# Optimization experiments

Hardware: AMD Instinct MI355X
Metric: run time of the kernel (lower is better)

The kernel has to match this reference:

```python
import jax, jax.numpy as jnp
import numpy as np

N_NODES = 40000
N_EDGES = 640000
D_FEAT = 128
HIDDEN = 128
N_GRAPHS = 512


def setup_inputs() -> dict:
    key = jax.random.key(0)
    ks = jax.random.split(key, 6)
    x = jax.random.normal(ks[0], (N_NODES, D_FEAT), dtype=jnp.float32)
    edge_index = jax.random.randint(ks[1], (2, N_EDGES), 0, N_NODES, dtype=jnp.int32)
    batch = jnp.sort(jax.random.randint(ks[2], (N_NODES,), 0, N_GRAPHS, dtype=jnp.int32))
    s1 = 1.0 / np.sqrt(D_FEAT)
    s2 = 1.0 / np.sqrt(HIDDEN)
    W1 = jax.random.normal(ks[3], (D_FEAT, HIDDEN), dtype=jnp.float32) * s1
    b1 = jnp.zeros((HIDDEN,), dtype=jnp.float32)
    W2 = jax.random.normal(ks[4], (HIDDEN, HIDDEN), dtype=jnp.float32) * s2
    b2 = jnp.zeros((HIDDEN,), dtype=jnp.float32)
    Wfc = jax.random.normal(ks[5], (HIDDEN, 1), dtype=jnp.float32) * s2
    bfc = jnp.zeros((1,), dtype=jnp.float32)
    return {"x": x, "edge_index": edge_index, "batch": batch,
            "W1": W1, "b1": b1, "W2": W2, "b2": b2, "Wfc": Wfc, "bfc": bfc}


def _gcn_conv(x, edge_index, W, b):
    # PyG GCNConv: linear transform, add self-loops, symmetric deg^{-1/2} norm,
    # scatter-add messages from row (source) to col (target), then bias.
    n = x.shape[0]
    h = x @ W  # [N, H]
    row, col = edge_index[0], edge_index[1]
    ones = jnp.ones_like(col, dtype=h.dtype)
    deg = 1.0 + jax.ops.segment_sum(ones, col, num_segments=n)  # self-loop included
    dinv = jax.lax.rsqrt(deg)  # [N]
    norm = dinv[row] * dinv[col]  # [E]
    msg = h[row] * norm[:, None]  # [E, H]
    out = jax.ops.segment_sum(msg, col, num_segments=n)
    out = out + h * (dinv * dinv)[:, None]  # self-loop contribution
    return out + b


def _mean_pool(x, batch, num_graphs):
    sums = jax.ops.segment_sum(x, batch, num_segments=num_graphs)
    cnt = jax.ops.segment_sum(jnp.ones((x.shape[0],), dtype=x.dtype), batch, num_segments=num_graphs)
    return sums / jnp.maximum(cnt, 1.0)[:, None]


def reference(x, edge_index, batch, W1, b1, W2, b2, Wfc, bfc):
    h = jax.nn.relu(_gcn_conv(x, edge_index, W1, b1))
    h = jax.nn.relu(_gcn_conv(h, edge_index, W2, b2))
    g = _mean_pool(h, batch, N_GRAPHS)  # [G, H]
    return g @ Wfc + bfc  # [G, 1]
```

## Files before the change

kernel.cpp:

```cpp
#include <hip/hip_runtime.h>

#define N_NODES 40000
#define N_EDGES 640000
#define NFEAT   128
#define N_GRAPHS 512
#define SCAN_NB 157


__global__ void edge_deg_int_kernel(const int* __restrict__ ei, int* __restrict__ degcnt, int E) {
    int e = blockIdx.x * blockDim.x + threadIdx.x;
    if (e < E) atomicAdd(&degcnt[ei[E + e]], 1);
}

__global__ void dinv_from_int_kernel(const int* __restrict__ degcnt, float* __restrict__ dinv, int n) {
    int i = blockIdx.x * blockDim.x + threadIdx.x;
    if (i < n) dinv[i] = rsqrtf(1.0f + (float)degcnt[i]);
}

__global__ void scan1_kernel(const int* __restrict__ in, int* __restrict__ out,
                             int* __restrict__ bsums, float* __restrict__ dinv, int n) {
    __shared__ int tmp[256];
    int t = threadIdx.x;
    int i = blockIdx.x * 256 + t;
    int v = (i < n) ? in[i] : 0;
    if (i < n) dinv[i] = rsqrtf(1.0f + (float)v);
    tmp[t] = v;
    __syncthreads();
    for (int off = 1; off < 256; off <<= 1) {
        int add = (t >= off) ? tmp[t - off] : 0;
        __syncthreads();
        tmp[t] += add;
        __syncthreads();
    }
    if (i < n) out[i] = tmp[t] - v;
    if (t == 255) bsums[blockIdx.x] = tmp[255];
}

__global__ void scan2_kernel(int* __restrict__ bsums, int nb) {
    __shared__ int tmp[256];
    int t = threadIdx.x;
    int v = (t < nb) ? bsums[t] : 0;
    tmp[t] = v;
    __syncthreads();
    for (int off = 1; off < 256; off <<= 1) {
        int add = (t >= off) ? tmp[t - off] : 0;
        __syncthreads();
        tmp[t] += add;
        __syncthreads();
    }
    if (t < nb) bsums[t] = tmp[t] - v;
}

__global__ void scan3_kernel(int* __restrict__ rowptr, const int* __restrict__ bsums,
                             int* __restrict__ cursor, int n, int E) {
    int i = blockIdx.x * 256 + threadIdx.x;
    if (i < n) {
        int v = rowptr[i] + bsums[blockIdx.x];
        rowptr[i] = v;
        cursor[i] = v;
    }
    if (i == 0) rowptr[n] = E;
}

template <typename IdxT>
__global__ void fill_kernel(const int* __restrict__ ei, int* __restrict__ cursor,
                            IdxT* __restrict__ csr, int E) {
    int e = blockIdx.x * blockDim.x + threadIdx.x;
    if (e < E) {
        int c = ei[E + e];
        int p = atomicAdd(&cursor[c], 1);
        csr[p] = (IdxT)ei[e];
    }
}

__global__ __launch_bounds__(256, 4) void gemm64_kernel(const float* __restrict__ X,
                                                        const float* __restrict__ W,
                                                        const float* __restrict__ dinv,
                                                        float* __restrict__ H) {
    __shared__ float Ws[128 * 64];
    const int colhalf = blockIdx.x & 1;
    const int tile    = blockIdx.x >> 1;

    for (int i = threadIdx.x; i < 2048; i += 256) {
        int k   = i >> 4;
        int cc4 = (i & 15) * 4;
        *(float4*)(Ws + k * 64 + cc4) = *(const float4*)(W + k * 128 + colhalf * 64 + cc4);
    }
    __syncthreads();

    const int rg = threadIdx.x >> 4;
    const int cg = threadIdx.x & 15;
    const int row0 = tile * 64 + rg * 4;
    const float* x0 = X + (size_t)row0 * NFEAT;

    float acc[4][4] = {};
    float4 xc[4], xn[4];
    #pragma unroll
    for (int i = 0; i < 4; i++) xc[i] = *(const float4*)(x0 + (size_t)i * NFEAT);

    #pragma unroll 4
    for (int k = 0; k < 128; k += 4) {
        const int kn = (k + 4) & 127;
        #pragma unroll
        for (int i = 0; i < 4; i++) xn[i] = *(const float4*)(x0 + (size_t)i * NFEAT + kn);

        float4 wv[4];
        #pragma unroll
        for (int m = 0; m < 4; m++) wv[m] = *(const float4*)(Ws + (k + m) * 64 + cg * 4);

        #pragma unroll
        for (int i = 0; i < 4; i++) {
            const float xi[4] = {xc[i].x, xc[i].y, xc[i].z, xc[i].w};
            #pragma unroll
            for (int m = 0; m < 4; m++) {
                acc[i][0] += xi[m] * wv[m].x;
                acc[i][1] += xi[m] * wv[m].y;
                acc[i][2] += xi[m] * wv[m].z;
                acc[i][3] += xi[m] * wv[m].w;
            }
        }
        #pragma unroll
        for (int i = 0; i < 4; i++) xc[i] = xn[i];
    }

    #pragma unroll
    for (int i = 0; i < 4; i++) {
        float dr = dinv[row0 + i];
        float4 o = {acc[i][0] * dr, acc[i][1] * dr, acc[i][2] * dr, acc[i][3] * dr};
        *(float4*)(H + (size_t)(row0 + i) * NFEAT + colhalf * 64 + cg * 4) = o;
    }
}

template <typename IdxT>
__global__ __launch_bounds__(256) void gather4_kernel(const int* __restrict__ rowptr,
                                                      const IdxT* __restrict__ csr,
                                                      const float* __restrict__ dinv,
                                                      const float* __restrict__ Ht,
                                                      const float* __restrict__ bias,
                                                      float* __restrict__ out, int n) {
    int gid  = blockIdx.x * blockDim.x + threadIdx.x;
    int node = gid >> 6;
    if (node >= n) return;
    int lane = threadIdx.x & 63;
    int half = lane >> 5;
    int f4   = (lane & 31) * 4;

    int start = rowptr[node];
    int end   = rowptr[node + 1];

    float4 a0 = {0.f, 0.f, 0.f, 0.f};
    float4 a1 = {0.f, 0.f, 0.f, 0.f};
    if (half == 0) a0 = *(const float4*)(Ht + (size_t)node * NFEAT + f4);

    int j = start + half;
    for (; j + 2 < end; j += 4) {
        int r0 = (int)csr[j];
        int r1 = (int)csr[j + 2];
        float4 v0 = *(const float4*)(Ht + (size_t)r0 * NFEAT + f4);
        float4 v1 = *(const float4*)(Ht + (size_t)r1 * NFEAT + f4);
        a0.x += v0.x; a0.y += v0.y; a0.z += v0.z; a0.w += v0.w;
        a1.x += v1.x; a1.y += v1.y; a1.z += v1.z; a1.w += v1.w;
    }
    if (j < end) {
        int r0 = (int)csr[j];
        float4 v0 = *(const float4*)(Ht + (size_t)r0 * NFEAT + f4);
        a0.x += v0.x; a0.y += v0.y; a0.z += v0.z; a0.w += v0.w;
    }
    a0.x += a1.x; a0.y += a1.y; a0.z += a1.z; a0.w += a1.w;

    a0.x += __shfl_xor(a0.x, 32, 64);
    a0.y += __shfl_xor(a0.y, 32, 64);
    a0.z += __shfl_xor(a0.z, 32, 64);
    a0.w += __shfl_xor(a0.w, 32, 64);

    if (half == 0) {
        float di  = dinv[node];
        float4 bb = *(const float4*)(bias + f4);
        float4 o;
        o.x = fmaxf(a0.x * di + bb.x, 0.0f);
        o.y = fmaxf(a0.y * di + bb.y, 0.0f);
        o.z = fmaxf(a0.z * di + bb.z, 0.0f);
        o.w = fmaxf(a0.w * di + bb.w, 0.0f);
        *(float4*)(out + (size_t)node * NFEAT + f4) = o;
    }
}

__global__ __launch_bounds__(256) void edge_scatter_kernel(const int* __restrict__ ei,
                                                           const float* __restrict__ dinv,
                                                           const float* __restrict__ H,
                                                           float* __restrict__ agg,
                                                           int E) {
    long long gid = (long long)blockIdx.x * blockDim.x + threadIdx.x;
    int e = (int)(gid >> 5);
    if (e >= E) return;
    int c4 = ((int)gid & 31) * 4;
    int r = ei[e];
    int c = ei[E + e];
    float norm = dinv[c];
    const float4 hv = *(const float4*)(H + (size_t)r * NFEAT + c4);
    float* dst = agg + (size_t)c * NFEAT + c4;
    atomicAdd(dst + 0, hv.x * norm);
    atomicAdd(dst + 1, hv.y * norm);
    atomicAdd(dst + 2, hv.z * norm);
    atomicAdd(dst + 3, hv.w * norm);
}

__global__ void post_kernel(float* __restrict__ agg, const float* __restrict__ H,
                            const float* __restrict__ dinv, const float* __restrict__ b,
                            int n) {
    int gid = blockIdx.x * blockDim.x + threadIdx.x;
    if (gid >= n * 32) return;
    int node = gid >> 5;
    int c4 = (gid & 31) * 4;
    float s = dinv[node];
    float4 a  = *(float4*)(agg + (size_t)gid * 4);
    float4 hv = *(const float4*)(H + (size_t)gid * 4);
    float4 bb = *(const float4*)(b + c4);
    float4 o;
    o.x = fmaxf(a.x + hv.x * s + bb.x, 0.0f);
    o.y = fmaxf(a.y + hv.y * s + bb.y, 0.0f);
    o.z = fmaxf(a.z + hv.z * s + bb.z, 0.0f);
    o.w = fmaxf(a.w + hv.w * s + bb.w, 0.0f);
    *(float4*)(agg + (size_t)gid * 4) = o;
}

__global__ __launch_bounds__(128) void pool_fc_kernel(const float* __restrict__ H,
                                                      const int* __restrict__ batch,
                                                      const float* __restrict__ Wfc,
                                                      const float* __restrict__ bfc,
                                                      float* __restrict__ out, int n) {
    int g = blockIdx.x;
    int tid = threadIdx.x;
    int lo = 0, hi = n;
    while (lo < hi) { int mid = (lo + hi) >> 1; if (batch[mid] < g) lo = mid + 1; else hi = mid; }
    int start = lo;
    hi = n;
    while (lo < hi) { int mid = (lo + hi) >> 1; if (batch[mid] < g + 1) lo = mid + 1; else hi = mid; }
    int end = lo;

    float acc = 0.0f;
    for (int nd = start; nd < end; ++nd) acc += H[(size_t)nd * NFEAT + tid];
    float cnt = (float)((end - start) > 0 ? (end - start) : 1);
    float v = (acc / cnt) * Wfc[tid];

    __shared__ float red[128];
    red[tid] = v;
    __syncthreads();
    #pragma unroll
    for (int s = 64; s > 0; s >>= 1) {
        if (tid < s) red[tid] += red[tid + s];
        __syncthreads();
    }
    if (tid == 0) out[g] = red[0] + bfc[0];
}

template <typename IdxT>
static void run_csr_path(const float* x, const int* ei, const int* batch,
                         const float* W1, const float* b1, const float* W2,
                         const float* b2, const float* Wfc, const float* bfc,
                         float* out, void* d_ws, hipStream_t stream) {
    char* ws = (char*)d_ws;
    const size_t fbytes = (size_t)N_NODES * NFEAT * sizeof(float);
    float* hbuf   = (float*)ws;
    float* obuf   = (float*)(ws + fbytes);
    IdxT*  csr    = (IdxT*)(ws + 2 * fbytes);
    char*  p      = ws + 2 * fbytes + ((size_t)N_EDGES * sizeof(IdxT) + 15) / 16 * 16;
    int*   rowptr = (int*)p;
    float* dinv   = (float*)(p + ((size_t)(N_NODES + 1) * 4 + 15) / 16 * 16);

    int* degcnt = (int*)obuf;
    int* cursor = (int*)obuf + N_NODES;
    int* bsums  = (int*)obuf + 2 * N_NODES;

    hipMemsetAsync(degcnt, 0, (size_t)N_NODES * sizeof(int), stream);
    edge_deg_int_kernel<<<N_EDGES / 256, 256, 0, stream>>>(ei, degcnt, N_EDGES);
    scan1_kernel<<<SCAN_NB, 256, 0, stream>>>(degcnt, rowptr, bsums, dinv, N_NODES);
    scan2_kernel<<<1, 256, 0, stream>>>(bsums, SCAN_NB);
    scan3_kernel<<<SCAN_NB, 256, 0, stream>>>(rowptr, bsums, cursor, N_NODES, N_EDGES);
    fill_kernel<IdxT><<<N_EDGES / 256, 256, 0, stream>>>(ei, cursor, csr, N_EDGES);

    gemm64_kernel<<<(N_NODES / 64) * 2, 256, 0, stream>>>(x, W1, dinv, hbuf);
    gather4_kernel<IdxT><<<(N_NODES * 64) / 256, 256, 0, stream>>>(rowptr, csr, dinv, hbuf, b1, obuf, N_NODES);

    gemm64_kernel<<<(N_NODES / 64) * 2, 256, 0, stream>>>(obuf, W2, dinv, hbuf);
    gather4_kernel<IdxT><<<(N_NODES * 64) / 256, 256, 0, stream>>>(rowptr, csr, dinv, hbuf, b2, obuf, N_NODES);

    pool_fc_kernel<<<N_GRAPHS, 128, 0, stream>>>(obuf, batch, Wfc, bfc, out, N_NODES);
}

extern "C" void kernel_launch(void* const* d_in, const int* in_sizes, int n_in,
                              void* d_out, int out_size, void* d_ws, size_t ws_size,
                              hipStream_t stream) {
    const float* x     = (const float*)d_in[0];
    const int*   ei    = (const int*)  d_in[1];
    const int*   batch = (const int*)  d_in[2];
    const float* W1    = (const float*)d_in[3];
    const float* b1    = (const float*)d_in[4];
    const float* W2    = (const float*)d_in[5];
    const float* b2    = (const float*)d_in[6];
    const float* Wfc   = (const float*)d_in[7];
    const float* bfc   = (const float*)d_in[8];
    float* out = (float*)d_out;

    const size_t fbytes = (size_t)N_NODES * NFEAT * sizeof(float);
    const size_t needA = 2 * fbytes + ((size_t)N_EDGES * 4 + 15) / 16 * 16
                       + ((size_t)(N_NODES + 1) * 4 + 15) / 16 * 16
                       + (size_t)N_NODES * 4;
    const size_t needB = 2 * fbytes + ((size_t)N_EDGES * 2 + 15) / 16 * 16
                       + ((size_t)(N_NODES + 1) * 4 + 15) / 16 * 16
                       + (size_t)N_NODES * 4;

    if (ws_size >= needA) {
        run_csr_path<int>(x, ei, batch, W1, b1, W2, b2, Wfc, bfc, out, d_ws, stream);
    } else if (ws_size >= needB) {
        run_csr_path<unsigned short>(x, ei, batch, W1, b1, W2, b2, Wfc, bfc, out, d_ws, stream);
    } else {
        float* ws   = (float*)d_ws;
        int*   degc = (int*)ws;
        float* dinv = ws + N_NODES;
        float* hbuf = ws + 2 * N_NODES;
        float* agg  = hbuf + (size_t)N_NODES * NFEAT;

        hipMemsetAsync(degc, 0, (size_t)N_NODES * sizeof(int), stream);
        edge_deg_int_kernel<<<N_EDGES / 256, 256, 0, stream>>>(ei, degc, N_EDGES);
        dinv_from_int_kernel<<<SCAN_NB, 256, 0, stream>>>(degc, dinv, N_NODES);

        hipMemsetAsync(agg, 0, fbytes, stream);
        gemm64_kernel<<<(N_NODES / 64) * 2, 256, 0, stream>>>(x, W1, dinv, hbuf);
        edge_scatter_kernel<<<(N_EDGES * 32) / 256, 256, 0, stream>>>(ei, dinv, hbuf, agg, N_EDGES);
        post_kernel<<<(N_NODES * 32) / 256, 256, 0, stream>>>(agg, hbuf, dinv, b1, N_NODES);

        gemm64_kernel<<<(N_NODES / 64) * 2, 256, 0, stream>>>(agg, W2, dinv, hbuf);
        hipMemsetAsync(agg, 0, fbytes, stream);
        edge_scatter_kernel<<<(N_EDGES * 32) / 256, 256, 0, stream>>>(ei, dinv, hbuf, agg, N_EDGES);
        post_kernel<<<(N_NODES * 32) / 256, 256, 0, stream>>>(agg, hbuf, dinv, b2, N_NODES);

        pool_fc_kernel<<<N_GRAPHS, 128, 0, stream>>>(agg, batch, Wfc, bfc, out, N_NODES);
    }
}
```

Before: 329.9 us.

## Slice gather by feature columns, pad CSR to 4, fuse pooling into final gather

Each node's CSR row is padded to a multiple of four with a dummy zero-row index, so the gather can read four neighbour indices at once with no tail loop. The gather is split into 8 feature slices of 16 columns, launched slice by slice so each slice's working set of H stays in cache. The second layer's gather now computes the per-node dot product with Wfc and accumulates it atomically, and a small per-node kernel turns that into the per-graph mean, so the second layer never writes its output. This costs extra kernels (batch histogram, padding, output init), a larger workspace, 16-lane scalar loads instead of float4, and float atomics whose summation order is not fixed.

Result: slower. 397.9 us (+20.6%).

```diff
diff --git a/kernel.cpp b/kernel.cpp
--- a/kernel.cpp
+++ b/kernel.cpp
@@ -5,11 +5,19 @@
 #define NFEAT   128
 #define N_GRAPHS 512
 #define SCAN_NB 157
+#define NSLICES 8
+#define SLICE_BLOCKS 2500
+#define EPAD_MAX (N_EDGES + 3 * N_NODES)
 
 
 __global__ void edge_deg_int_kernel(const int* __restrict__ ei, int* __restrict__ degcnt, int E) {
     int e = blockIdx.x * blockDim.x + threadIdx.x;
     if (e < E) atomicAdd(&degcnt[ei[E + e]], 1);
+}
+
+__global__ void batch_hist_kernel(const int* __restrict__ batch, int* __restrict__ gcnt, int n) {
+    int i = blockIdx.x * blockDim.x + threadIdx.x;
+    if (i < n) atomicAdd(&gcnt[batch[i]], 1);
 }
 
 __global__ void dinv_from_int_kernel(const int* __restrict__ degcnt, float* __restrict__ dinv, int n) {
@@ -22,9 +30,10 @@
     __shared__ int tmp[256];
     int t = threadIdx.x;
     int i = blockIdx.x * 256 + t;
-    int v = (i < n) ? in[i] : 0;
-    if (i < n) dinv[i] = rsqrtf(1.0f + (float)v);
-    tmp[t] = v;
+    int deg = (i < n) ? in[i] : 0;
+    if (i < n) dinv[i] = rsqrtf(1.0f + (float)deg);
+    int vp = (i < n) ? ((deg + 3) & ~3) : 0;
+    tmp[t] = vp;
     __syncthreads();
     for (int off = 1; off < 256; off <<= 1) {
         int add = (t >= off) ? tmp[t - off] : 0;
@@ -32,7 +41,7 @@
         tmp[t] += add;
         __syncthreads();
     }
-    if (i < n) out[i] = tmp[t] - v;
+    if (i < n) out[i] = tmp[t] - vp;
     if (t == 255) bsums[blockIdx.x] = tmp[255];
 }
 
@@ -52,14 +61,15 @@
 }
 
 __global__ void scan3_kernel(int* __restrict__ rowptr, const int* __restrict__ bsums,
-                             int* __restrict__ cursor, int n, int E) {
+                             int* __restrict__ cursor, const int* __restrict__ degcnt,
+                             int n) {
     int i = blockIdx.x * 256 + threadIdx.x;
     if (i < n) {
         int v = rowptr[i] + bsums[blockIdx.x];
         rowptr[i] = v;
         cursor[i] = v;
-    }
-    if (i == 0) rowptr[n] = E;
+        if (i == n - 1) rowptr[n] = v + ((degcnt[i] + 3) & ~3);
+    }
 }
 
 template <typename IdxT>
@@ -71,6 +81,21 @@
         int p = atomicAdd(&cursor[c], 1);
         csr[p] = (IdxT)ei[e];
     }
+}
+
+template <typename IdxT>
+__global__ void pad_kernel(const int* __restrict__ rowptr, const int* __restrict__ cursor,
+                           IdxT* __restrict__ csr, int n) {
+    int i = blockIdx.x * blockDim.x + threadIdx.x;
+    if (i < n) {
+        int end = rowptr[i + 1];
+        for (int p = cursor[i]; p < end; ++p) csr[p] = (IdxT)N_NODES;
+    }
+}
+
+__global__ void out_init_kernel(float* __restrict__ out, const float* __restrict__ bfc, int g) {
+    int i = blockIdx.x * blockDim.x + threadIdx.x;
+    if (i < g) out[i] = bfc[0];
 }
 
 __global__ __launch_bounds__(256, 4) void gemm64_kernel(const float* __restrict__ X,
@@ -131,57 +156,57 @@
     }
 }
 
-template <typename IdxT>
-__global__ __launch_bounds__(256) void gather4_kernel(const int* __restrict__ rowptr,
-                                                      const IdxT* __restrict__ csr,
-                                                      const float* __restrict__ dinv,
-                                                      const float* __restrict__ Ht,
-                                                      const float* __restrict__ bias,
-                                                      float* __restrict__ out, int n) {
-    int gid  = blockIdx.x * blockDim.x + threadIdx.x;
-    int node = gid >> 6;
-    if (node >= n) return;
-    int lane = threadIdx.x & 63;
-    int half = lane >> 5;
-    int f4   = (lane & 31) * 4;
-
-    int start = rowptr[node];
-    int end   = rowptr[node + 1];
-
-    float4 a0 = {0.f, 0.f, 0.f, 0.f};
-    float4 a1 = {0.f, 0.f, 0.f, 0.f};
-    if (half == 0) a0 = *(const float4*)(Ht + (size_t)node * NFEAT + f4);
-
-    int j = start + half;
-    for (; j + 2 < end; j += 4) {
-        int r0 = (int)csr[j];
-        int r1 = (int)csr[j + 2];
-        float4 v0 = *(const float4*)(Ht + (size_t)r0 * NFEAT + f4);
-        float4 v1 = *(const float4*)(Ht + (size_t)r1 * NFEAT + f4);
-        a0.x += v0.x; a0.y += v0.y; a0.z += v0.z; a0.w += v0.w;
-        a1.x += v1.x; a1.y += v1.y; a1.z += v1.z; a1.w += v1.w;
-    }
-    if (j < end) {
-        int r0 = (int)csr[j];
-        float4 v0 = *(const float4*)(Ht + (size_t)r0 * NFEAT + f4);
-        a0.x += v0.x; a0.y += v0.y; a0.z += v0.z; a0.w += v0.w;
-    }
-    a0.x += a1.x; a0.y += a1.y; a0.z += a1.z; a0.w += a1.w;
-
-    a0.x += __shfl_xor(a0.x, 32, 64);
-    a0.y += __shfl_xor(a0.y, 32, 64);
-    a0.z += __shfl_xor(a0.z, 32, 64);
-    a0.w += __shfl_xor(a0.w, 32, 64);
-
-    if (half == 0) {
-        float di  = dinv[node];
-        float4 bb = *(const float4*)(bias + f4);
-        float4 o;
-        o.x = fmaxf(a0.x * di + bb.x, 0.0f);
-        o.y = fmaxf(a0.y * di + bb.y, 0.0f);
-        o.z = fmaxf(a0.z * di + bb.z, 0.0f);
-        o.w = fmaxf(a0.w * di + bb.w, 0.0f);
-        *(float4*)(out + (size_t)node * NFEAT + f4) = o;
+template <typename IdxT, typename IdxV, bool FUSE_POOL>
+__global__ __launch_bounds__(256) void gather_sliced_kernel(
+        const int* __restrict__ rowptr, const IdxT* __restrict__ csr,
+        const float* __restrict__ dinv, const float* __restrict__ Ht,
+        const float* __restrict__ bias, float* __restrict__ out,
+        const float* __restrict__ Wfc, float* __restrict__ nodedot) {
+    const int slice = blockIdx.x / SLICE_BLOCKS;
+    const int nblk  = blockIdx.x % SLICE_BLOCKS;
+    const int node  = nblk * 16 + (threadIdx.x >> 4);
+    const int lane16 = threadIdx.x & 15;
+    const int f = slice * 16 + lane16;
+
+    const int start = rowptr[node];
+    const int end   = rowptr[node + 1];
+
+    float acc0 = Ht[(size_t)node * NFEAT + f];
+    float acc1 = 0.0f, acc2 = 0.0f, acc3 = 0.0f;
+
+    for (int j = start; j < end; j += 4) {
+        IdxV rr = *(const IdxV*)(csr + j);
+        int r0 = (int)rr.x, r1 = (int)rr.y, r2 = (int)rr.z, r3 = (int)rr.w;
+        acc0 += Ht[(size_t)r0 * NFEAT + f];
+        acc1 += Ht[(size_t)r1 * NFEAT + f];
+        acc2 += Ht[(size_t)r2 * NFEAT + f];
+        acc3 += Ht[(size_t)r3 * NFEAT + f];
+    }
+    float v = ((acc0 + acc1) + (acc2 + acc3)) * dinv[node] + bias[f];
+    v = fmaxf(v, 0.0f);
+
+    if (!FUSE_POOL) {
+        out[(size_t)node * NFEAT + f] = v;
+    } else {
+        float d = v * Wfc[f];
+        d += __shfl_xor(d, 1, 64);
+        d += __shfl_xor(d, 2, 64);
+        d += __shfl_xor(d, 4, 64);
+        d += __shfl_xor(d, 8, 64);
+        if (lane16 == 0) atomicAdd(&nodedot[node], d);
+    }
+}
+
+__global__ void pool_final_kernel(const float* __restrict__ nodedot,
+                                  const int* __restrict__ batch,
+                                  const int* __restrict__ gcnt,
+                                  float* __restrict__ out, int n) {
+    int i = blockIdx.x * blockDim.x + threadIdx.x;
+    if (i < n) {
+        int g = batch[i];
+        int c = gcnt[g];
+        float cf = (float)(c > 0 ? c : 1);
+        atomicAdd(&out[g], nodedot[i] / cf);
     }
 }
 
@@ -254,38 +279,48 @@
     if (tid == 0) out[g] = red[0] + bfc[0];
 }
 
-template <typename IdxT>
+template <typename IdxT, typename IdxV>
 static void run_csr_path(const float* x, const int* ei, const int* batch,
                          const float* W1, const float* b1, const float* W2,
                          const float* b2, const float* Wfc, const float* bfc,
                          float* out, void* d_ws, hipStream_t stream) {
     char* ws = (char*)d_ws;
-    const size_t fbytes = (size_t)N_NODES * NFEAT * sizeof(float);
+    const size_t fbytes = (size_t)(N_NODES + 1) * NFEAT * sizeof(float);
     float* hbuf   = (float*)ws;
     float* obuf   = (float*)(ws + fbytes);
     IdxT*  csr    = (IdxT*)(ws + 2 * fbytes);
-    char*  p      = ws + 2 * fbytes + ((size_t)N_EDGES * sizeof(IdxT) + 15) / 16 * 16;
-    int*   rowptr = (int*)p;
-    float* dinv   = (float*)(p + ((size_t)(N_NODES + 1) * 4 + 15) / 16 * 16);
+    char*  p      = ws + 2 * fbytes + ((size_t)EPAD_MAX * sizeof(IdxT) + 15) / 16 * 16;
+    int*   rowptr = (int*)p;                         p += ((size_t)(N_NODES + 1) * 4 + 15) / 16 * 16;
+    float* dinv   = (float*)p;                       p += ((size_t)N_NODES * 4 + 15) / 16 * 16;
+    int*   gcnt   = (int*)p;
 
     int* degcnt = (int*)obuf;
     int* cursor = (int*)obuf + N_NODES;
     int* bsums  = (int*)obuf + 2 * N_NODES;
+    float* nodedot = (float*)obuf;
 
     hipMemsetAsync(degcnt, 0, (size_t)N_NODES * sizeof(int), stream);
+    hipMemsetAsync(gcnt, 0, (size_t)N_GRAPHS * sizeof(int), stream);
     edge_deg_int_kernel<<<N_EDGES / 256, 256, 0, stream>>>(ei, degcnt, N_EDGES);
+    batch_hist_kernel<<<SCAN_NB, 256, 0, stream>>>(batch, gcnt, N_NODES);
     scan1_kernel<<<SCAN_NB, 256, 0, stream>>>(degcnt, rowptr, bsums, dinv, N_NODES);
     scan2_kernel<<<1, 256, 0, stream>>>(bsums, SCAN_NB);
-    scan3_kernel<<<SCAN_NB, 256, 0, stream>>>(rowptr, bsums, cursor, N_NODES, N_EDGES);
+    scan3_kernel<<<SCAN_NB, 256, 0, stream>>>(rowptr, bsums, cursor, degcnt, N_NODES);
     fill_kernel<IdxT><<<N_EDGES / 256, 256, 0, stream>>>(ei, cursor, csr, N_EDGES);
+    pad_kernel<IdxT><<<SCAN_NB, 256, 0, stream>>>(rowptr, cursor, csr, N_NODES);
+    out_init_kernel<<<2, 256, 0, stream>>>(out, bfc, N_GRAPHS);
+    hipMemsetAsync(hbuf + (size_t)N_NODES * NFEAT, 0, NFEAT * sizeof(float), stream);
 
     gemm64_kernel<<<(N_NODES / 64) * 2, 256, 0, stream>>>(x, W1, dinv, hbuf);
-    gather4_kernel<IdxT><<<(N_NODES * 64) / 256, 256, 0, stream>>>(rowptr, csr, dinv, hbuf, b1, obuf, N_NODES);
+    gather_sliced_kernel<IdxT, IdxV, false><<<NSLICES * SLICE_BLOCKS, 256, 0, stream>>>(
+        rowptr, csr, dinv, hbuf, b1, obuf, nullptr, nullptr);
 
     gemm64_kernel<<<(N_NODES / 64) * 2, 256, 0, stream>>>(obuf, W2, dinv, hbuf);
-    gather4_kernel<IdxT><<<(N_NODES * 64) / 256, 256, 0, stream>>>(rowptr, csr, dinv, hbuf, b2, obuf, N_NODES);
-
-    pool_fc_kernel<<<N_GRAPHS, 128, 0, stream>>>(obuf, batch, Wfc, bfc, out, N_NODES);
+    hipMemsetAsync(nodedot, 0, (size_t)N_NODES * sizeof(float), stream);
+    gather_sliced_kernel<IdxT, IdxV, true><<<NSLICES * SLICE_BLOCKS, 256, 0, stream>>>(
+        rowptr, csr, dinv, hbuf, b2, nullptr, Wfc, nodedot);
+
+    pool_final_kernel<<<SCAN_NB, 256, 0, stream>>>(nodedot, batch, gcnt, out, N_NODES);
 }
 
 extern "C" void kernel_launch(void* const* d_in, const int* in_sizes, int n_in,
@@ -302,36 +337,36 @@
     const float* bfc   = (const float*)d_in[8];
     float* out = (float*)d_out;
 
-    const size_t fbytes = (size_t)N_NODES * NFEAT * sizeof(float);
-    const size_t needA = 2 * fbytes + ((size_t)N_EDGES * 4 + 15) / 16 * 16
-                       + ((size_t)(N_NODES + 1) * 4 + 15) / 16 * 16
-                       + (size_t)N_NODES * 4;
-    const size_t needB = 2 * fbytes + ((size_t)N_EDGES * 2 + 15) / 16 * 16
-                       + ((size_t)(N_NODES + 1) * 4 + 15) / 16 * 16
-                       + (size_t)N_NODES * 4;
+    const size_t fbytes = (size_t)(N_NODES + 1) * NFEAT * sizeof(float);
+    const size_t tail   = ((size_t)(N_NODES + 1) * 4 + 15) / 16 * 16
+                        + ((size_t)N_NODES * 4 + 15) / 16 * 16
+                        + (size_t)N_GRAPHS * 4;
+    const size_t needA = 2 * fbytes + ((size_t)EPAD_MAX * 4 + 15) / 16 * 16 + tail;
+    const size_t needB = 2 * fbytes + ((size_t)EPAD_MAX * 2 + 15) / 16 * 16 + tail;
 
     if (ws_size >= needA) {
-        run_csr_path<int>(x, ei, batch, W1, b1, W2, b2, Wfc, bfc, out, d_ws, stream);
+        run_csr_path<int, int4>(x, ei, batch, W1, b1, W2, b2, Wfc, bfc, out, d_ws, stream);
     } else if (ws_size >= needB) {
-        run_csr_path<unsigned short>(x, ei, batch, W1, b1, W2, b2, Wfc, bfc, out, d_ws, stream);
+        run_csr_path<unsigned short, ushort4>(x, ei, batch, W1, b1, W2, b2, Wfc, bfc, out, d_ws, stream);
     } else {
         float* ws   = (float*)d_ws;
         int*   degc = (int*)ws;
         float* dinv = ws + N_NODES;
         float* hbuf = ws + 2 * N_NODES;
         float* agg  = hbuf + (size_t)N_NODES * NFEAT;
+        const size_t fb2 = (size_t)N_NODES * NFEAT * sizeof(float);
 
         hipMemsetAsync(degc, 0, (size_t)N_NODES * sizeof(int), stream);
         edge_deg_int_kernel<<<N_EDGES / 256, 256, 0, stream>>>(ei, degc, N_EDGES);
         dinv_from_int_kernel<<<SCAN_NB, 256, 0, stream>>>(degc, dinv, N_NODES);
 
-        hipMemsetAsync(agg, 0, fbytes, stream);
+        hipMemsetAsync(agg, 0, fb2, stream);
         gemm64_kernel<<<(N_NODES / 64) * 2, 256, 0, stream>>>(x, W1, dinv, hbuf);
         edge_scatter_kernel<<<(N_EDGES * 32) / 256, 256, 0, stream>>>(ei, dinv, hbuf, agg, N_EDGES);
         post_kernel<<<(N_NODES * 32) / 256, 256, 0, stream>>>(agg, hbuf, dinv, b1, N_NODES);
 
         gemm64_kernel<<<(N_NODES / 64) * 2, 256, 0, stream>>>(agg, W2, dinv, hbuf);
-        hipMemsetAsync(agg, 0, fbytes, stream);
+        hipMemsetAsync(agg, 0, fb2, stream);
         edge_scatter_kernel<<<(N_EDGES * 32) / 256, 256, 0, stream>>>(ei, dinv, hbuf, agg, N_EDGES);
         post_kernel<<<(N_NODES * 32) / 256, 256, 0, stream>>>(agg, hbuf, dinv, b2, N_NODES);
 
```
